# Kernel tuning notes

Hardware: AMD Instinct MI355X
Metric: run time of the kernel (lower is better)

## Reference

```python
import jax, jax.numpy as jnp
import numpy as np

WSZ = 8
HEADS = 8
FILTER_RATE = 0.3
EPS = 1e-5


def layer_norm(x, w, b):
    mu = x.mean(-1, keepdims=True)
    var = ((x - mu) ** 2).mean(-1, keepdims=True)
    return (x - mu) * jax.lax.rsqrt(var + EPS) * w + b


def setup_inputs() -> dict:
    key = jax.random.key(0)
    ks = jax.random.split(key, 8)
    B, C, H, W = 2, 256, 512, 512
    C2 = 2 * C
    s = 0.02
    return {
        "feature_map": jax.random.normal(ks[0], (B, C, H, W), jnp.float32),
        "uncertain_map": jax.random.uniform(ks[1], (B, H, W), jnp.float32),
        "norm_w": jnp.ones((C,), jnp.float32),
        "norm_b": jnp.zeros((C,), jnp.float32),
        "lin0_w": jax.random.normal(ks[2], (C, C2), jnp.float32) * s,
        "lin0_b": jnp.zeros((C2,), jnp.float32),
        "qkv0_w": jax.random.normal(ks[3], (C2, 3 * C2), jnp.float32) * s,
        "lin1_w": jax.random.normal(ks[4], (C2, C2), jnp.float32) * s,
        "lin1_b": jnp.zeros((C2,), jnp.float32),
        "qkv1_w": jax.random.normal(ks[5], (C2, 3 * C2), jnp.float32) * s,
        "proj_w": jax.random.normal(ks[6], (C2, C), jnp.float32) * s,
        "proj_b": jnp.zeros((C,), jnp.float32),
    }


def _window_attn(xf, qkv_w, scale, winsz, C2):
    # xf: (N, winsz, C2)
    qkv = (xf @ qkv_w).reshape(-1, winsz, 3, HEADS, C2 // HEADS)
    q, k, v = qkv[:, :, 0], qkv[:, :, 1], qkv[:, :, 2]  # (N, winsz, H, dh)
    a = jnp.einsum("nqhd,nkhd->nhqk", q, k) * scale
    a = jax.nn.softmax(a, axis=-1)
    o = jnp.einsum("nhqk,nkhd->nqhd", a, v).reshape(-1, winsz, C2)
    return xf + o


def reference(feature_map, uncertain_map, norm_w, norm_b, lin0_w, lin0_b,
              qkv0_w, lin1_w, lin1_b, qkv1_w, proj_w, proj_b):
    B, C, H, W = feature_map.shape
    wsz = WSZ
    nH, nW = H // wsz, W // wsz
    nWin, winsz = nH * nW, wsz * wsz
    nWF = int(nWin * FILTER_RATE)
    C2 = 2 * C
    scale = (C // HEADS) ** -0.5  # module uses C//num_heads, not C2//num_heads

    # window partition
    x = jnp.transpose(feature_map, (0, 2, 3, 1))  # B H W C
    win_x = x.reshape(B, nH, wsz, nW, wsz, C).transpose(0, 1, 3, 2, 4, 5)
    win_x = win_x.reshape(B * nWin, winsz, C)
    win_unc = uncertain_map.reshape(B, nH, wsz, nW, wsz).transpose(0, 1, 3, 2, 4)
    win_unc = win_unc.reshape(B, nWin, winsz)

    # topk window selection by mean uncertainty
    score = win_unc.mean(-1)  # (B, nWin)
    _, idx = jax.lax.top_k(score, nWF)  # (B, nWF)
    flat_idx = (idx + jnp.arange(B)[:, None] * nWin).reshape(-1)  # (B*nWF,)

    xw = win_x[flat_idx]  # gather: (B*nWF, winsz, C)
    xn = layer_norm(xw, norm_w, norm_b)

    # local branch: repeat 0
    xf = jax.nn.gelu(xn @ lin0_w + lin0_b, approximate=False)
    xf = _window_attn(xf, qkv0_w, scale, winsz, C2)
    # repeat 1
    xf = xf + jax.nn.gelu(xf @ lin1_w + lin1_b, approximate=False)
    xf = _window_attn(xf, qkv1_w, scale, winsz, C2)

    out_f = xn + jax.nn.gelu(xf @ proj_w + proj_b, approximate=False)

    # scatter-add back into unnormalized windows
    win_x = win_x.at[flat_idx].add(out_f)

    x = win_x.reshape(B, nH, nW, wsz, wsz, C).transpose(0, 1, 3, 2, 4, 5)
    x = x.reshape(B, H, W, C)
    return jnp.transpose(x, (0, 3, 1, 2))
```

## Files before the change

kernel.cpp:

```cpp
#include <hip/hip_runtime.h>
#include <math.h>

typedef unsigned short u16;
typedef unsigned int   u32;
typedef __attribute__((ext_vector_type(8))) short bf16x8;
typedef __attribute__((ext_vector_type(4))) float f32x4;

#define DEV static __device__ __forceinline__

DEV u16 f2b(float f) {
  union { float f; u32 u; } v; v.f = f;
  u32 r = v.u + 0x7FFFu + ((v.u >> 16) & 1u);
  return (u16)(r >> 16);
}
DEV float b2f(u16 h) {
  union { u32 u; float f; } v; v.u = ((u32)h) << 16;
  return v.f;
}
DEV float gelu_f(float x) { return 0.5f * x * (1.0f + erff(x * 0.70710678118654752f)); }

DEV void gload16(const u16* g, u16* l) {
  __builtin_amdgcn_global_load_lds(
      (const __attribute__((address_space(1))) void*)g,
      (__attribute__((address_space(3))) void*)l, 16, 0, 0);
}

__global__ void k_transpose_w(const float* __restrict__ src, u16* __restrict__ dst,
                              int K, int N) {
  long t = (long)blockIdx.x * 256 + threadIdx.x;
  if (t >= (long)K * N) return;
  int n = (int)(t / K), k = (int)(t % K);
  dst[t] = f2b(src[(long)k * N + n]);
}

__global__ void k_scores(const float* __restrict__ unc, float* __restrict__ scores) {
  int id = blockIdx.x * 256 + threadIdx.x;
  if (id >= 8192) return;
  int b = id >> 12, win = id & 4095;
  int h0 = (win >> 6) << 3, w0 = (win & 63) << 3;
  float r[8] = {0.f,0.f,0.f,0.f,0.f,0.f,0.f,0.f};
  for (int i = 0; i < 8; ++i) {
    long base = ((long)(b * 512 + h0 + i)) * 512 + w0;
    #pragma unroll
    for (int j = 0; j < 8; ++j) r[j] += unc[base + j];
  }
  float s = ((r[0] + r[1]) + (r[2] + r[3])) + ((r[4] + r[5]) + (r[6] + r[7]));
  scores[id] = s * (1.0f / 64.0f);
}

__global__ __launch_bounds__(1024) void k_topk(
    const float* __restrict__ scores, int* __restrict__ row2win,
    int* __restrict__ win2row, int nWF) {
  __shared__ float ls[4096];
  __shared__ int   li[4096];
  const int b = blockIdx.x;
  const int tid = threadIdx.x;
  for (int i = tid; i < 4096; i += 1024) {
    ls[i] = scores[b * 4096 + i];
    li[i] = i;
    win2row[b * 4096 + i] = -1;
  }
  __syncthreads();
  for (int k = 2; k <= 4096; k <<= 1) {
    for (int j = k >> 1; j > 0; j >>= 1) {
      for (int t = tid; t < 2048; t += 1024) {
        int i = ((t / j) * (j << 1)) + (t % j);
        int ixj = i + j;
        bool up = ((i & k) == 0);
        float sa = ls[i], sb = ls[ixj];
        int ia = li[i], ib = li[ixj];
        bool g = (sa > sb) || (sa == sb && ia < ib);
        if (g != up) { ls[i] = sb; ls[ixj] = sa; li[i] = ib; li[ixj] = ia; }
      }
      __syncthreads();
    }
  }
  for (int r = tid; r < nWF; r += 1024) {
    int win = li[r];
    row2win[b * nWF + r] = (b << 12) | win;
    win2row[b * 4096 + win] = b * nWF + r;
  }
}

__global__ __launch_bounds__(256) void k_gather_ln(
    const float* __restrict__ fm, const float* __restrict__ nw,
    const float* __restrict__ nb, const int* __restrict__ row2win,
    u16* __restrict__ xn, int winStart) {
  __shared__ float sx[64 * 256];
  const int tid = threadIdx.x;
  const int rw = row2win[winStart + blockIdx.x];
  const int b = rw >> 12, win = rw & 4095;
  const int h0 = (win >> 6) << 3, w0 = (win & 63) << 3;
  {
    const int c8 = tid >> 3, h = tid & 7;
    #pragma unroll
    for (int cc = 0; cc < 8; ++cc) {
      const int c = cc * 32 + c8;
      long base = ((long)(b * 256 + c) * 512 + h0 + h) * 512 + w0;
      float4 v0 = *(const float4*)(fm + base);
      float4 v1 = *(const float4*)(fm + base + 4);
      float vv[8] = {v0.x, v0.y, v0.z, v0.w, v1.x, v1.y, v1.z, v1.w};
      #pragma unroll
      for (int j = 0; j < 8; ++j) {
        int tok = h * 8 + j;
        sx[tok * 256 + (c ^ ((tok & 15) << 1))] = vv[j];
      }
    }
  }
  __syncthreads();
  const int tok = tid >> 2, g = tid & 3;
  const int swz = (tok & 15) << 1;
  float sum = 0.f;
  for (int q = 0; q < 64; ++q) sum += sx[tok * 256 + ((g * 64 + q) ^ swz)];
  sum += __shfl_xor(sum, 1);
  sum += __shfl_xor(sum, 2);
  const float mu = sum * (1.0f / 256.0f);
  float s2 = 0.f;
  for (int q = 0; q < 64; ++q) {
    float d = sx[tok * 256 + ((g * 64 + q) ^ swz)] - mu;
    s2 += d * d;
  }
  s2 += __shfl_xor(s2, 1);
  s2 += __shfl_xor(s2, 2);
  const float rs = rsqrtf(s2 * (1.0f / 256.0f) + 1e-5f);
  long obase = ((long)blockIdx.x * 64 + tok) * 256 + g * 64;
  for (int q8 = 0; q8 < 8; ++q8) {
    u16 tmp[8];
    #pragma unroll
    for (int e = 0; e < 8; ++e) {
      int c = g * 64 + q8 * 8 + e;
      float v = (sx[tok * 256 + (c ^ swz)] - mu) * rs * nw[c] + nb[c];
      tmp[e] = f2b(v);
    }
    *(ulonglong2*)(xn + obase + q8 * 8) = *(const ulonglong2*)tmp;
  }
}

template <int EPI, int NT, int KD>
__global__ __launch_bounds__(512, 2) void k_gemm256(
    const u16* __restrict__ A, const u16* __restrict__ Bt,
    const float* __restrict__ bias, const u16* __restrict__ Res,
    u16* __restrict__ Y, int N) {
  __shared__ __attribute__((aligned(16))) u16 S[65536];
  const int tid = threadIdx.x;
  const int l = tid & 63, wid = tid >> 6;
  const int wm = wid >> 2, wn = wid & 3;

  const int nwg = gridDim.x;
  const int d = blockIdx.x;
  const int xcd = d & 7, j = d >> 3;
  const int q = nwg >> 3, r8 = nwg & 7;
  const int wrk = (xcd < r8 ? xcd * (q + 1) : r8 * (q + 1) + (xcd - r8) * q) + j;
  const int tm = wrk / NT, tn = wrk % NT;

  const int srow = wid * 8 + (l >> 3);
  const int k0b = ((l & 7) << 4) ^ ((l >> 3) << 4);
  const u16* gA = A + (long)(tm * 256 + srow) * KD + (k0b >> 1);
  const u16* gB = Bt + (long)(tn * 256 + srow) * KD + (k0b >> 1);
  char* ldsS = (char*)S + wid * 1024 + l * 16;
  const char* Sb = (const char*)S;

  f32x4 acc[8][4] = {};
  bf16x8 bfrag[4][2];
  bf16x8 af[2][2];

#define STG(T, ISB, H) do { \
    const u16* g_ = (ISB) ? gB : gA; \
    char* lp_ = ldsS + ((T) & 1) * 65536 + (ISB) * 32768 + (H) * 16384; \
    gload16(g_ + (long)((H) * 128) * KD + (long)(T) * 64, (u16*)lp_); \
    gload16(g_ + (long)((H) * 128 + 64) * KD + (long)(T) * 64, (u16*)(lp_ + 8192)); \
  } while (0)

#define DS_B(T) do { \
    _Pragma("unroll") for (int ni_ = 0; ni_ < 4; ++ni_) { \
      const int r_ = wn * 64 + ni_ * 16 + (l & 15); \
      _Pragma("unroll") for (int kk_ = 0; kk_ < 2; ++kk_) { \
        const int kb_ = kk_ * 64 + ((l >> 4) << 4); \
        bfrag[ni_][kk_] = *(const bf16x8*)(Sb + ((T) & 1) * 65536 + 32768 + r_ * 128 + (kb_ ^ ((r_ & 7) << 4))); \
      } } \
  } while (0)

#define DS_A(T, Q) do { \
    _Pragma("unroll") for (int m2_ = 0; m2_ < 2; ++m2_) { \
      const int r_ = wm * 128 + (2 * (Q) + m2_) * 16 + (l & 15); \
      _Pragma("unroll") for (int kk_ = 0; kk_ < 2; ++kk_) { \
        const int kb_ = kk_ * 64 + ((l >> 4) << 4); \
        af[m2_][kk_] = *(const bf16x8*)(Sb + ((T) & 1) * 65536 + r_ * 128 + (kb_ ^ ((r_ & 7) << 4))); \
      } } \
  } while (0)

#define MFMA16(Q) do { \
    _Pragma("unroll") for (int m2_ = 0; m2_ < 2; ++m2_) \
      _Pragma("unroll") for (int ni_ = 0; ni_ < 4; ++ni_) \
        _Pragma("unroll") for (int kk_ = 0; kk_ < 2; ++kk_) \
          acc[2 * (Q) + m2_][ni_] = __builtin_amdgcn_mfma_f32_16x16x32_bf16( \
              af[m2_][kk_], bfrag[ni_][kk_], acc[2 * (Q) + m2_][ni_], 0, 0, 0); \
  } while (0)

#define BAR_MFMA(Q) do { \
    __builtin_amdgcn_s_barrier(); \
    asm volatile("s_waitcnt lgkmcnt(0)" ::: "memory"); \
    __builtin_amdgcn_sched_barrier(0); \
    __builtin_amdgcn_s_setprio(1); \
    MFMA16(Q); \
    __builtin_amdgcn_s_setprio(0); \
  } while (0)

#define PH_END() do { \
    __builtin_amdgcn_s_barrier(); \
    __builtin_amdgcn_sched_barrier(0); \
  } while (0)

  STG(0, 0, 0); STG(0, 0, 1); STG(0, 1, 0); STG(0, 1, 1);
  STG(1, 0, 0); STG(1, 0, 1); STG(1, 1, 0); STG(1, 1, 1);
  asm volatile("s_waitcnt vmcnt(8)" ::: "memory");
  __builtin_amdgcn_s_barrier();
  __builtin_amdgcn_sched_barrier(0);

  constexpr int nIter = KD >> 7;
  for (int i = 0; i < nIter; ++i) {
    const int t0 = 2 * i, t1 = 2 * i + 1;
    const bool more = (i + 1 < nIter);
    DS_B(t0); DS_A(t0, 0);
    if (i > 0) STG(t1, 0, 0);
    BAR_MFMA(0); PH_END();
    DS_A(t0, 1);
    if (i > 0) STG(t1, 0, 1);
    if (more) STG(t0 + 2, 1, 0);
    BAR_MFMA(1); PH_END();
    DS_A(t0, 2);
    if (more) STG(t0 + 2, 1, 1);
    BAR_MFMA(2); PH_END();
    DS_A(t0, 3);
    BAR_MFMA(3);
    if (more) { asm volatile("s_waitcnt vmcnt(4)" ::: "memory"); }
    else      { asm volatile("s_waitcnt vmcnt(0)" ::: "memory"); }
    PH_END();
    DS_B(t1); DS_A(t1, 0);
    if (more) STG(t0 + 2, 0, 0);
    BAR_MFMA(0); PH_END();
    DS_A(t1, 1);
    if (more) STG(t0 + 2, 0, 1);
    BAR_MFMA(1); PH_END();
    DS_A(t1, 2);
    if (more) STG(t1 + 2, 1, 0);
    BAR_MFMA(2); PH_END();
    DS_A(t1, 3);
    if (more) STG(t1 + 2, 1, 1);
    BAR_MFMA(3);
    if (more) { asm volatile("s_waitcnt vmcnt(4)" ::: "memory"); }
    PH_END();
  }

  if (EPI == 3) {
    float bv[4];
    #pragma unroll
    for (int ni = 0; ni < 4; ++ni)
      bv[ni] = bias[tn * 256 + wn * 64 + ni * 16 + (l & 15)];
    #pragma unroll
    for (int mi = 0; mi < 8; ++mi) {
      #pragma unroll
      for (int r = 0; r < 4; ++r) {
        const int ml = wm * 128 + mi * 16 + ((l >> 4) << 2) + r;
        #pragma unroll
        for (int ni = 0; ni < 4; ++ni) {
          const int nl = wn * 64 + ni * 16 + (l & 15);
          float v = gelu_f(acc[mi][ni][r] + bv[ni]);
          S[nl * 256 + ((((ml >> 3) ^ ((nl & 7) << 2)) << 3) | (ml & 7))] = f2b(v);
        }
      }
    }
    asm volatile("s_waitcnt lgkmcnt(0)" ::: "memory");
    __builtin_amdgcn_s_barrier();
    #pragma unroll
    for (int rd = 0; rd < 16; ++rd) {
      const int id = rd * 512 + tid;
      const int nl = id >> 5, c8 = id & 31;
      ulonglong2 val = *(const ulonglong2*)(S + nl * 256 + ((c8 ^ ((nl & 7) << 2)) << 3));
      u16 tv[8];
      *(ulonglong2*)tv = val;
      const long mg = (long)tm * 256 + c8 * 8;
      const int ng = tn * 256 + nl;
      #pragma unroll
      for (int e = 0; e < 8; ++e) tv[e] = f2b(b2f(tv[e]) + b2f(Res[(mg + e) * N + ng]));
      const long row = (mg >> 6);
      *(ulonglong2*)(Y + (row * 256 + ng) * 64 + (c8 & 7) * 8) = *(const ulonglong2*)tv;
    }
  } else {
    float bv[4];
    if (EPI == 1 || EPI == 2) {
      #pragma unroll
      for (int ni = 0; ni < 4; ++ni)
        bv[ni] = bias[tn * 256 + wn * 64 + ni * 16 + (l & 15)];
    }
    #pragma unroll
    for (int sw = 0; sw < 4; ++sw) {
      #pragma unroll
      for (int mi2 = 0; mi2 < 2; ++mi2) {
        const int mi = 2 * sw + mi2;
        const int lr0 = wm * 32 + mi2 * 16 + ((l >> 4) << 2);
        #pragma unroll
        for (int r = 0; r < 4; ++r) {
          const int lrr = lr0 + r;
          #pragma unroll
          for (int ni = 0; ni < 4; ++ni) {
            float v = acc[mi][ni][r];
            if (EPI == 1 || EPI == 2) v = gelu_f(v + bv[ni]);
            const int col = wn * 64 + ni * 16 + (l & 15);
            S[lrr * 256 + ((((col >> 3) ^ (lrr & 7)) << 3) | (col & 7))] = f2b(v);
          }
        }
      }
      asm volatile("s_waitcnt lgkmcnt(0)" ::: "memory");
      __builtin_amdgcn_s_barrier();
      const int lr2 = tid >> 3;
      const long m = (long)tm * 256 + (lr2 >> 5) * 128 + sw * 32 + (lr2 & 31);
      #pragma unroll
      for (int rd = 0; rd < 4; ++rd) {
        const int chunk = rd * 8 + (tid & 7);
        ulonglong2 val = *(const ulonglong2*)(S + lr2 * 256 + ((chunk ^ (lr2 & 7)) << 3));
        const int n = tn * 256 + chunk * 8;
        if (EPI == 2) {
          u16 tv[8], rv[8];
          *(ulonglong2*)tv = val;
          *(ulonglong2*)rv = *(const ulonglong2*)(Res + m * N + n);
          #pragma unroll
          for (int e = 0; e < 8; ++e) tv[e] = f2b(b2f(tv[e]) + b2f(rv[e]));
          val = *(const ulonglong2*)tv;
        }
        if (EPI == 4) {
          const long win = m >> 6;
          const int t_ = n >> 9, h_ = (n >> 6) & 7, d0 = n & 63;
          *(ulonglong2*)(Y + ((((win * 8 + h_) * 3 + t_) * 64 + (m & 63)) * 64 + d0)) = val;
        } else {
          *(ulonglong2*)(Y + m * N + n) = val;
        }
      }
      if (sw < 3) {
        __builtin_amdgcn_s_barrier();
      }
    }
  }
#undef STG
#undef DS_B
#undef DS_A
#undef MFMA16
#undef BAR_MFMA
#undef PH_END
}

__global__ __launch_bounds__(256) void k_attn(
    const u16* __restrict__ qkv, u16* __restrict__ xf) {
  __shared__ __attribute__((aligned(16))) u16 sq[64 * 64];
  __shared__ __attribute__((aligned(16))) u16 sk[64 * 64];
  __shared__ __attribute__((aligned(16))) u16 sv[64 * 64];
  __shared__ __attribute__((aligned(16))) u16 sp[64 * 64];
  const int tid = threadIdx.x;
  const int l = tid & 63, w = tid >> 6;
  const int wloc = blockIdx.x >> 3, h = blockIdx.x & 7;
  const long tokbase = (long)wloc * 64;
  const u16* base = qkv + (long)blockIdx.x * 12288;

  #pragma unroll
  for (int rd = 0; rd < 6; ++rd) {
    const int cid = rd * 256 + tid;
    ulonglong2 v16 = *(const ulonglong2*)(base + (long)cid * 8);
    const int t = (cid >> 3) & 63, d0 = (cid & 7) << 3;
    if (rd < 2) {
      *(ulonglong2*)((char*)sq + t * 128 + ((d0 * 2) ^ ((t & 7) << 4))) = v16;
    } else if (rd < 4) {
      *(ulonglong2*)((char*)sk + t * 128 + ((d0 * 2) ^ ((t & 7) << 4))) = v16;
    } else {
      u16 vv[8];
      *(ulonglong2*)vv = v16;
      #pragma unroll
      for (int e = 0; e < 8; ++e) {
        int r = d0 + e;
        *(u16*)((char*)sv + r * 128 + ((t * 2) ^ ((r & 7) << 4))) = vv[e];
      }
    }
  }
  __syncthreads();

  f32x4 accs[4] = {};
  #pragma unroll
  for (int ks = 0; ks < 2; ++ks) {
    int kb = ks * 64 + ((l >> 4) << 4);
    int ra = w * 16 + (l & 15);
    bf16x8 aq = *(const bf16x8*)((char*)sq + ra * 128 + (kb ^ ((ra & 7) << 4)));
    #pragma unroll
    for (int cf = 0; cf < 4; ++cf) {
      int rb = cf * 16 + (l & 15);
      bf16x8 bk = *(const bf16x8*)((char*)sk + rb * 128 + (kb ^ ((rb & 7) << 4)));
      accs[cf] = __builtin_amdgcn_mfma_f32_16x16x32_bf16(aq, bk, accs[cf], 0, 0, 0);
    }
  }
  const float scale = 0.17677669529663687f;
  float pv[4][4];
  #pragma unroll
  for (int r = 0; r < 4; ++r) {
    float m = -1e30f;
    #pragma unroll
    for (int cf = 0; cf < 4; ++cf) {
      pv[cf][r] = accs[cf][r] * scale;
      m = fmaxf(m, pv[cf][r]);
    }
    for (int off = 1; off < 16; off <<= 1) m = fmaxf(m, __shfl_xor(m, off));
    float s = 0.f;
    #pragma unroll
    for (int cf = 0; cf < 4; ++cf) { pv[cf][r] = __expf(pv[cf][r] - m); s += pv[cf][r]; }
    for (int off = 1; off < 16; off <<= 1) s += __shfl_xor(s, off);
    float inv = 1.0f / s;
    #pragma unroll
    for (int cf = 0; cf < 4; ++cf) pv[cf][r] *= inv;
  }
  #pragma unroll
  for (int cf = 0; cf < 4; ++cf)
    #pragma unroll
    for (int r = 0; r < 4; ++r) {
      int pr = w * 16 + ((l >> 4) << 2) + r, pc = cf * 16 + (l & 15);
      *(u16*)((char*)sp + pr * 128 + ((pc * 2) ^ ((pr & 7) << 4))) = f2b(pv[cf][r]);
    }
  __syncthreads();

  f32x4 acco[4] = {};
  #pragma unroll
  for (int ks = 0; ks < 2; ++ks) {
    int kb = ks * 64 + ((l >> 4) << 4);
    int ra = w * 16 + (l & 15);
    bf16x8 ap = *(const bf16x8*)((char*)sp + ra * 128 + (kb ^ ((ra & 7) << 4)));
    #pragma unroll
    for (int cf = 0; cf < 4; ++cf) {
      int rb = cf * 16 + (l & 15);
      bf16x8 bvv = *(const bf16x8*)((char*)sv + rb * 128 + (kb ^ ((rb & 7) << 4)));
      acco[cf] = __builtin_amdgcn_mfma_f32_16x16x32_bf16(ap, bvv, acco[cf], 0, 0, 0);
    }
  }
  #pragma unroll
  for (int cf = 0; cf < 4; ++cf)
    #pragma unroll
    for (int r = 0; r < 4; ++r) {
      int orow = w * 16 + ((l >> 4) << 2) + r, ocol = cf * 16 + (l & 15);
      *(u16*)((char*)sq + orow * 128 + ((ocol * 2) ^ ((orow & 7) << 4))) = f2b(acco[cf][r]);
    }
  __syncthreads();
  {
    const int row = tid >> 2, c32 = tid & 3;
    const long gaddr = (tokbase + row) * 512 + h * 64 + c32 * 16;
    #pragma unroll
    for (int hh = 0; hh < 2; ++hh) {
      const int colb = c32 * 32 + hh * 16;
      ulonglong2 ov = *(const ulonglong2*)((char*)sq + row * 128 + (colb ^ ((row & 7) << 4)));
      ulonglong2 xv = *(const ulonglong2*)(xf + gaddr + hh * 8);
      u16 o16[8], x16[8];
      *(ulonglong2*)o16 = ov;
      *(ulonglong2*)x16 = xv;
      #pragma unroll
      for (int e = 0; e < 8; ++e) x16[e] = f2b(b2f(x16[e]) + b2f(o16[e]));
      *(ulonglong2*)(xf + gaddr + hh * 8) = *(const ulonglong2*)x16;
    }
  }
}

__global__ __launch_bounds__(256) void k_assemble(
    const float* __restrict__ fm, const u16* __restrict__ out_f,
    const int* __restrict__ win2row, float* __restrict__ out) {
  const int tid = threadIdx.x;
  const int bq = blockIdx.x;
  const int hw = bq & 63, c = (bq >> 6) & 255, b = bq >> 14;
  const int w0 = (tid & 127) << 2;
  const int hlo = tid >> 7;
  const int win = hw * 64 + (w0 >> 3);
  const int r = win2row[b * 4096 + win];
  const u16* ofb = out_f + ((long)(r < 0 ? 0 : r) * 256 + c) * 64 + (w0 & 7);
  const long base = ((long)(b * 256 + c) * 512 + hw * 8) * 512 + w0;
  #pragma unroll
  for (int jj = 0; jj < 4; ++jj) {
    const int h = jj * 2 + hlo;
    float4 v = *(const float4*)(fm + base + (long)h * 512);
    if (r >= 0) {
      ushort4 ov = *(const ushort4*)(ofb + h * 8);
      v.x += b2f(ov.x);
      v.y += b2f(ov.y);
      v.z += b2f(ov.z);
      v.w += b2f(ov.w);
    }
    *(float4*)(out + base + (long)h * 512) = v;
  }
}

extern "C" void kernel_launch(void* const* d_in, const int* in_sizes, int n_in,
                              void* d_out, int out_size, void* d_ws, size_t ws_size,
                              hipStream_t stream) {
  const float* fm     = (const float*)d_in[0];
  const float* unc    = (const float*)d_in[1];
  const float* nw     = (const float*)d_in[2];
  const float* nb     = (const float*)d_in[3];
  const float* w_lin0 = (const float*)d_in[4];
  const float* b_lin0 = (const float*)d_in[5];
  const float* w_qkv0 = (const float*)d_in[6];
  const float* w_lin1 = (const float*)d_in[7];
  const float* b_lin1 = (const float*)d_in[8];
  const float* w_qkv1 = (const float*)d_in[9];
  const float* w_proj = (const float*)d_in[10];
  const float* b_proj = (const float*)d_in[11];
  float* out = (float*)d_out;

  const int nWF = 1228, totWin = 2456;
  const long totTok = (long)totWin * 64;

  char* p = (char*)d_ws;
  auto alloc = [&](size_t bytes) {
    char* r = p;
    p += (bytes + 255) & ~(size_t)255;
    return r;
  };
  float* scores = (float*)alloc(8192 * 4);
  int* win2row  = (int*)alloc(8192 * 4);
  int* row2win  = (int*)alloc(totWin * 4);
  u16* wT       = (u16*)alloc((size_t)2097152 * 2);
  u16* out_f    = (u16*)alloc((size_t)(totTok + 256) * 256 * 2);
  size_t persist = (size_t)(p - (char*)d_ws);

  int wpc = totWin;
  {
    const int cands[6] = {1, 2, 4, 8, 16, 32};
    for (int ci = 0; ci < 6; ++ci) {
      int n = cands[ci];
      int wp = ((totWin + n - 1) / n + 3) & ~3;
      size_t mc = (size_t)wp * 64;
      size_t need = persist + 4096 +
                    ((mc * 256 * 2 + 255) & ~(size_t)255) +
                    2 * ((mc * 512 * 2 + 255) & ~(size_t)255) +
                    ((mc * 1536 * 2 + 255) & ~(size_t)255);
      if (need <= ws_size) { wpc = wp; break; }
    }
  }
  long mcap = (long)wpc * 64;
  u16* xn   = (u16*)alloc((size_t)mcap * 256 * 2);
  u16* xfa  = (u16*)alloc((size_t)mcap * 512 * 2);
  u16* xfb  = (u16*)alloc((size_t)mcap * 512 * 2);
  u16* qkvb = (u16*)alloc((size_t)mcap * 1536 * 2);

  u16* wT_lin0 = wT;
  u16* wT_qkv0 = wT + 131072;
  u16* wT_lin1 = wT + 917504;
  u16* wT_qkv1 = wT + 1179648;
  u16* wT_proj = wT + 1966080;
  k_transpose_w<<<(131072 + 255) / 256, 256, 0, stream>>>(w_lin0, wT_lin0, 256, 512);
  k_transpose_w<<<(786432 + 255) / 256, 256, 0, stream>>>(w_qkv0, wT_qkv0, 512, 1536);
  k_transpose_w<<<(262144 + 255) / 256, 256, 0, stream>>>(w_lin1, wT_lin1, 512, 512);
  k_transpose_w<<<(786432 + 255) / 256, 256, 0, stream>>>(w_qkv1, wT_qkv1, 512, 1536);
  k_transpose_w<<<(131072 + 255) / 256, 256, 0, stream>>>(w_proj, wT_proj, 512, 256);

  k_scores<<<32, 256, 0, stream>>>(unc, scores);
  k_topk<<<2, 1024, 0, stream>>>(scores, row2win, win2row, nWF);

  for (int w0 = 0; w0 < totWin; w0 += wpc) {
    int rem = totWin - w0;
    int wn = (wpc < rem) ? wpc : rem;
    int mT = wn / 4;
    k_gather_ln<<<wn, 256, 0, stream>>>(fm, nw, nb, row2win, xn, w0);
    k_gemm256<1, 2, 256><<<mT * 2, 512, 0, stream>>>(xn, wT_lin0, b_lin0, nullptr, xfa, 512);
    k_gemm256<4, 6, 512><<<mT * 6, 512, 0, stream>>>(xfa, wT_qkv0, nullptr, nullptr, qkvb, 1536);
    k_attn<<<wn * 8, 256, 0, stream>>>(qkvb, xfa);
    k_gemm256<2, 2, 512><<<mT * 2, 512, 0, stream>>>(xfa, wT_lin1, b_lin1, xfa, xfb, 512);
    k_gemm256<4, 6, 512><<<mT * 6, 512, 0, stream>>>(xfb, wT_qkv1, nullptr, nullptr, qkvb, 1536);
    k_attn<<<wn * 8, 256, 0, stream>>>(qkvb, xfb);
    k_gemm256<3, 1, 512><<<mT * 1, 512, 0, stream>>>(xfb, wT_proj, b_proj, xn,
                                                     out_f + (long)w0 * 16384, 256);
  }
  k_assemble<<<32768, 256, 0, stream>>>(fm, out_f, win2row, out);
}
```

Baseline: 1.759 ms.

## Process paired N-tiles per GEMM block with in-loop epilogue and trim attention LDS

The GEMM kernel gains a PAIR parameter so each workgroup computes two adjacent 256-wide N tiles back to back. The K-tile pipeline runs continuously across both tiles, and the epilogue for the first tile runs inside the loop using a separate LDS buffer E, so prefetch of the next tile's operands can overlap with it. The A-tile is re-read from global for the second N tile, and the grid is halved. The attention kernel drops its separate P buffer by reusing the K buffer after QK^T, and defers the V transpose into LDS until after the softmax, holding V in registers. This lowers LDS use at the cost of an extra barrier. The larger GEMM LDS footprint may reduce occupancy, and fewer workgroups may underfill the GPU.

```diff
diff --git a/kernel.cpp b/kernel.cpp
--- a/kernel.cpp
+++ b/kernel.cpp
@@ -136,12 +136,16 @@
   }
 }
 
-template <int EPI, int NT, int KD>
+template <int EPI, int NT, int KD, int PAIR>
 __global__ __launch_bounds__(512, 2) void k_gemm256(
     const u16* __restrict__ A, const u16* __restrict__ Bt,
     const float* __restrict__ bias, const u16* __restrict__ Res,
     u16* __restrict__ Y, int N) {
+  constexpr int NKT = KD / 64;
+  constexpr int LG_NKT = (KD == 512) ? 3 : 2;
+  constexpr int NIP = KD / 128;
   __shared__ __attribute__((aligned(16))) u16 S[65536];
+  __shared__ __attribute__((aligned(16))) u16 E[16384];
   const int tid = threadIdx.x;
   const int l = tid & 63, wid = tid >> 6;
   const int wm = wid >> 2, wn = wid & 3;
@@ -151,12 +155,13 @@
   const int xcd = d & 7, j = d >> 3;
   const int q = nwg >> 3, r8 = nwg & 7;
   const int wrk = (xcd < r8 ? xcd * (q + 1) : r8 * (q + 1) + (xcd - r8) * q) + j;
-  const int tm = wrk / NT, tn = wrk % NT;
+  constexpr int NTP = NT / PAIR;
+  const int tm = wrk / NTP, tp = wrk % NTP;
 
   const int srow = wid * 8 + (l >> 3);
   const int k0b = ((l & 7) << 4) ^ ((l >> 3) << 4);
-  const u16* gA = A + (long)(tm * 256 + srow) * KD + (k0b >> 1);
-  const u16* gB = Bt + (long)(tn * 256 + srow) * KD + (k0b >> 1);
+  const int vko = k0b >> 1;
+  const u16* gA = A + (long)(tm * 256 + srow) * KD + vko;
   char* ldsS = (char*)S + wid * 1024 + l * 16;
   const char* Sb = (const char*)S;
 
@@ -164,11 +169,18 @@
   bf16x8 bfrag[4][2];
   bf16x8 af[2][2];
 
-#define STG(T, ISB, H) do { \
-    const u16* g_ = (ISB) ? gB : gA; \
-    char* lp_ = ldsS + ((T) & 1) * 65536 + (ISB) * 32768 + (H) * 16384; \
-    gload16(g_ + (long)((H) * 128) * KD + (long)(T) * 64, (u16*)lp_); \
-    gload16(g_ + (long)((H) * 128 + 64) * KD + (long)(T) * 64, (u16*)(lp_ + 8192)); \
+#define STG(G, ISB, H) do { \
+    const int ktg_ = (G) & (NKT - 1); \
+    const u16* g_; \
+    if (ISB) { \
+      const int tng_ = tp * PAIR + ((G) >> LG_NKT); \
+      g_ = Bt + (long)(tng_ * 256 + srow) * KD + vko; \
+    } else { \
+      g_ = gA; \
+    } \
+    char* lp_ = ldsS + ((G) & 1) * 65536 + (ISB) * 32768 + (H) * 16384; \
+    gload16(g_ + (long)((H) * 128) * KD + ktg_ * 64, (u16*)lp_); \
+    gload16(g_ + (long)((H) * 128 + 64) * KD + ktg_ * 64, (u16*)(lp_ + 8192)); \
   } while (0)
 
 #define DS_B(T) do { \
@@ -217,7 +229,7 @@
   __builtin_amdgcn_s_barrier();
   __builtin_amdgcn_sched_barrier(0);
 
-  constexpr int nIter = KD >> 7;
+  constexpr int nIter = (PAIR * NKT) >> 1;
   for (int i = 0; i < nIter; ++i) {
     const int t0 = 2 * i, t1 = 2 * i + 1;
     const bool more = (i + 1 < nIter);
@@ -250,95 +262,101 @@
     BAR_MFMA(3);
     if (more) { asm volatile("s_waitcnt vmcnt(4)" ::: "memory"); }
     PH_END();
-  }
-
-  if (EPI == 3) {
-    float bv[4];
-    #pragma unroll
-    for (int ni = 0; ni < 4; ++ni)
-      bv[ni] = bias[tn * 256 + wn * 64 + ni * 16 + (l & 15)];
-    #pragma unroll
-    for (int mi = 0; mi < 8; ++mi) {
-      #pragma unroll
-      for (int r = 0; r < 4; ++r) {
-        const int ml = wm * 128 + mi * 16 + ((l >> 4) << 2) + r;
+
+    if (((i + 1) & (NIP - 1)) == 0) {
+      const int tn = tp * PAIR + ((i + 1) / NIP - 1);
+      if (EPI == 3) {
+        float bv[4];
         #pragma unroll
-        for (int ni = 0; ni < 4; ++ni) {
-          const int nl = wn * 64 + ni * 16 + (l & 15);
-          float v = gelu_f(acc[mi][ni][r] + bv[ni]);
-          S[nl * 256 + ((((ml >> 3) ^ ((nl & 7) << 2)) << 3) | (ml & 7))] = f2b(v);
+        for (int ni = 0; ni < 4; ++ni)
+          bv[ni] = bias[tn * 256 + wn * 64 + ni * 16 + (l & 15)];
+        #pragma unroll
+        for (int mi = 0; mi < 8; ++mi) {
+          #pragma unroll
+          for (int r = 0; r < 4; ++r) {
+            const int ml = wm * 128 + mi * 16 + ((l >> 4) << 2) + r;
+            #pragma unroll
+            for (int ni = 0; ni < 4; ++ni) {
+              const int nl = wn * 64 + ni * 16 + (l & 15);
+              float v = gelu_f(acc[mi][ni][r] + bv[ni]);
+              S[nl * 256 + ((((ml >> 3) ^ ((nl & 7) << 2)) << 3) | (ml & 7))] = f2b(v);
+            }
+          }
+        }
+        asm volatile("s_waitcnt lgkmcnt(0)" ::: "memory");
+        __builtin_amdgcn_s_barrier();
+        #pragma unroll
+        for (int rd = 0; rd < 16; ++rd) {
+          const int id = rd * 512 + tid;
+          const int nl = id >> 5, c8 = id & 31;
+          ulonglong2 val = *(const ulonglong2*)(S + nl * 256 + ((c8 ^ ((nl & 7) << 2)) << 3));
+          u16 tv[8];
+          *(ulonglong2*)tv = val;
+          const long mg = (long)tm * 256 + c8 * 8;
+          const int ng = tn * 256 + nl;
+          #pragma unroll
+          for (int e = 0; e < 8; ++e) tv[e] = f2b(b2f(tv[e]) + b2f(Res[(mg + e) * N + ng]));
+          const long row = (mg >> 6);
+          *(ulonglong2*)(Y + (row * 256 + ng) * 64 + (c8 & 7) * 8) = *(const ulonglong2*)tv;
+        }
+      } else {
+        float bv[4];
+        if (EPI == 1 || EPI == 2) {
+          #pragma unroll
+          for (int ni = 0; ni < 4; ++ni)
+            bv[ni] = bias[tn * 256 + wn * 64 + ni * 16 + (l & 15)];
+        }
+        #pragma unroll
+        for (int sw = 0; sw < 4; ++sw) {
+          #pragma unroll
+          for (int mi2 = 0; mi2 < 2; ++mi2) {
+            const int mi = 2 * sw + mi2;
+            const int lr0 = wm * 32 + mi2 * 16 + ((l >> 4) << 2);
+            #pragma unroll
+            for (int r = 0; r < 4; ++r) {
+              const int lrr = lr0 + r;
+              #pragma unroll
+              for (int ni = 0; ni < 4; ++ni) {
+                float v = acc[mi][ni][r];
+                if (EPI == 1 || EPI == 2) v = gelu_f(v + bv[ni]);
+                const int col = wn * 64 + ni * 16 + (l & 15);
+                E[lrr * 256 + ((((col >> 3) ^ (lrr & 7)) << 3) | (col & 7))] = f2b(v);
+              }
+            }
+          }
+          asm volatile("s_waitcnt lgkmcnt(0)" ::: "memory");
+          __builtin_amdgcn_s_barrier();
+          const int lr2 = tid >> 3;
+          const long m = (long)tm * 256 + (lr2 >> 5) * 128 + sw * 32 + (lr2 & 31);
+          #pragma unroll
+          for (int rd = 0; rd < 4; ++rd) {
+            const int chunk = rd * 8 + (tid & 7);
+            ulonglong2 val = *(const ulonglong2*)(E + lr2 * 256 + ((chunk ^ (lr2 & 7)) << 3));
+            const int n = tn * 256 + chunk * 8;
+            if (EPI == 2) {
+              u16 tv[8], rv[8];
+              *(ulonglong2*)tv = val;
+              *(ulonglong2*)rv = *(const ulonglong2*)(Res + m * N + n);
+              #pragma unroll
+              for (int e = 0; e < 8; ++e) tv[e] = f2b(b2f(tv[e]) + b2f(rv[e]));
+              val = *(const ulonglong2*)tv;
+            }
+            if (EPI == 4) {
+              const long win = m >> 6;
+              const int t_ = n >> 9, h_ = (n >> 6) & 7, d0 = n & 63;
+              *(ulonglong2*)(Y + ((((win * 8 + h_) * 3 + t_) * 64 + (m & 63)) * 64 + d0)) = val;
+            } else {
+              *(ulonglong2*)(Y + m * N + n) = val;
+            }
+          }
+          __builtin_amdgcn_s_barrier();
         }
       }
-    }
-    asm volatile("s_waitcnt lgkmcnt(0)" ::: "memory");
-    __builtin_amdgcn_s_barrier();
-    #pragma unroll
-    for (int rd = 0; rd < 16; ++rd) {
-      const int id = rd * 512 + tid;
-      const int nl = id >> 5, c8 = id & 31;
-      ulonglong2 val = *(const ulonglong2*)(S + nl * 256 + ((c8 ^ ((nl & 7) << 2)) << 3));
-      u16 tv[8];
-      *(ulonglong2*)tv = val;
-      const long mg = (long)tm * 256 + c8 * 8;
-      const int ng = tn * 256 + nl;
       #pragma unroll
-      for (int e = 0; e < 8; ++e) tv[e] = f2b(b2f(tv[e]) + b2f(Res[(mg + e) * N + ng]));
-      const long row = (mg >> 6);
-      *(ulonglong2*)(Y + (row * 256 + ng) * 64 + (c8 & 7) * 8) = *(const ulonglong2*)tv;
-    }
-  } else {
-    float bv[4];
-    if (EPI == 1 || EPI == 2) {
-      #pragma unroll
-      for (int ni = 0; ni < 4; ++ni)
-        bv[ni] = bias[tn * 256 + wn * 64 + ni * 16 + (l & 15)];
-    }
-    #pragma unroll
-    for (int sw = 0; sw < 4; ++sw) {
-      #pragma unroll
-      for (int mi2 = 0; mi2 < 2; ++mi2) {
-        const int mi = 2 * sw + mi2;
-        const int lr0 = wm * 32 + mi2 * 16 + ((l >> 4) << 2);
+      for (int mi = 0; mi < 8; ++mi)
         #pragma unroll
-        for (int r = 0; r < 4; ++r) {
-          const int lrr = lr0 + r;
-          #pragma unroll
-          for (int ni = 0; ni < 4; ++ni) {
-            float v = acc[mi][ni][r];
-            if (EPI == 1 || EPI == 2) v = gelu_f(v + bv[ni]);
-            const int col = wn * 64 + ni * 16 + (l & 15);
-            S[lrr * 256 + ((((col >> 3) ^ (lrr & 7)) << 3) | (col & 7))] = f2b(v);
-          }
-        }
-      }
-      asm volatile("s_waitcnt lgkmcnt(0)" ::: "memory");
-      __builtin_amdgcn_s_barrier();
-      const int lr2 = tid >> 3;
-      const long m = (long)tm * 256 + (lr2 >> 5) * 128 + sw * 32 + (lr2 & 31);
-      #pragma unroll
-      for (int rd = 0; rd < 4; ++rd) {
-        const int chunk = rd * 8 + (tid & 7);
-        ulonglong2 val = *(const ulonglong2*)(S + lr2 * 256 + ((chunk ^ (lr2 & 7)) << 3));
-        const int n = tn * 256 + chunk * 8;
-        if (EPI == 2) {
-          u16 tv[8], rv[8];
-          *(ulonglong2*)tv = val;
-          *(ulonglong2*)rv = *(const ulonglong2*)(Res + m * N + n);
-          #pragma unroll
-          for (int e = 0; e < 8; ++e) tv[e] = f2b(b2f(tv[e]) + b2f(rv[e]));
-          val = *(const ulonglong2*)tv;
-        }
-        if (EPI == 4) {
-          const long win = m >> 6;
-          const int t_ = n >> 9, h_ = (n >> 6) & 7, d0 = n & 63;
-          *(ulonglong2*)(Y + ((((win * 8 + h_) * 3 + t_) * 64 + (m & 63)) * 64 + d0)) = val;
-        } else {
-          *(ulonglong2*)(Y + m * N + n) = val;
-        }
-      }
-      if (sw < 3) {
-        __builtin_amdgcn_s_barrier();
-      }
+        for (int ni = 0; ni < 4; ++ni)
+          acc[mi][ni] = (f32x4){0.f, 0.f, 0.f, 0.f};
     }
   }
 #undef STG
@@ -354,31 +372,23 @@
   __shared__ __attribute__((aligned(16))) u16 sq[64 * 64];
   __shared__ __attribute__((aligned(16))) u16 sk[64 * 64];
   __shared__ __attribute__((aligned(16))) u16 sv[64 * 64];
-  __shared__ __attribute__((aligned(16))) u16 sp[64 * 64];
   const int tid = threadIdx.x;
   const int l = tid & 63, w = tid >> 6;
   const int wloc = blockIdx.x >> 3, h = blockIdx.x & 7;
   const long tokbase = (long)wloc * 64;
   const u16* base = qkv + (long)blockIdx.x * 12288;
 
-  #pragma unroll
-  for (int rd = 0; rd < 6; ++rd) {
+  ulonglong2 vreg[2];
+  vreg[0] = *(const ulonglong2*)(base + (long)(1024 + tid) * 8);
+  vreg[1] = *(const ulonglong2*)(base + (long)(1280 + tid) * 8);
+  #pragma unroll
+  for (int rd = 0; rd < 4; ++rd) {
     const int cid = rd * 256 + tid;
     ulonglong2 v16 = *(const ulonglong2*)(base + (long)cid * 8);
     const int t = (cid >> 3) & 63, d0 = (cid & 7) << 3;
-    if (rd < 2) {
-      *(ulonglong2*)((char*)sq + t * 128 + ((d0 * 2) ^ ((t & 7) << 4))) = v16;
-    } else if (rd < 4) {
-      *(ulonglong2*)((char*)sk + t * 128 + ((d0 * 2) ^ ((t & 7) << 4))) = v16;
-    } else {
-      u16 vv[8];
-      *(ulonglong2*)vv = v16;
-      #pragma unroll
-      for (int e = 0; e < 8; ++e) {
-        int r = d0 + e;
-        *(u16*)((char*)sv + r * 128 + ((t * 2) ^ ((r & 7) << 4))) = vv[e];
-      }
-    }
+    const int sbyte = t * 128 + ((d0 * 2) ^ ((t & 7) << 4));
+    if (rd < 2) *(ulonglong2*)((char*)sq + sbyte) = v16;
+    else        *(ulonglong2*)((char*)sk + sbyte) = v16;
   }
   __syncthreads();
 
@@ -395,6 +405,8 @@
       accs[cf] = __builtin_amdgcn_mfma_f32_16x16x32_bf16(aq, bk, accs[cf], 0, 0, 0);
     }
   }
+  __syncthreads();
+
   const float scale = 0.17677669529663687f;
   float pv[4][4];
   #pragma unroll
@@ -419,8 +431,20 @@
     #pragma unroll
     for (int r = 0; r < 4; ++r) {
       int pr = w * 16 + ((l >> 4) << 2) + r, pc = cf * 16 + (l & 15);
-      *(u16*)((char*)sp + pr * 128 + ((pc * 2) ^ ((pr & 7) << 4))) = f2b(pv[cf][r]);
-    }
+      *(u16*)((char*)sk + pr * 128 + ((pc * 2) ^ ((pr & 7) << 4))) = f2b(pv[cf][r]);
+    }
+  #pragma unroll
+  for (int rv = 0; rv < 2; ++rv) {
+    const int cid = (4 + rv) * 256 + tid;
+    const int t = (cid >> 3) & 63, d0 = (cid & 7) << 3;
+    u16 vv[8];
+    *(ulonglong2*)vv = vreg[rv];
+    #pragma unroll
+    for (int e = 0; e < 8; ++e) {
+      int r = d0 + e;
+      *(u16*)((char*)sv + r * 128 + ((t * 2) ^ ((r & 7) << 4))) = vv[e];
+    }
+  }
   __syncthreads();
 
   f32x4 acco[4] = {};
@@ -428,7 +452,7 @@
   for (int ks = 0; ks < 2; ++ks) {
     int kb = ks * 64 + ((l >> 4) << 4);
     int ra = w * 16 + (l & 15);
-    bf16x8 ap = *(const bf16x8*)((char*)sp + ra * 128 + (kb ^ ((ra & 7) << 4)));
+    bf16x8 ap = *(const bf16x8*)((char*)sk + ra * 128 + (kb ^ ((ra & 7) << 4)));
     #pragma unroll
     for (int cf = 0; cf < 4; ++cf) {
       int rb = cf * 16 + (l & 15);
@@ -561,14 +585,14 @@
     int wn = (wpc < rem) ? wpc : rem;
     int mT = wn / 4;
     k_gather_ln<<<wn, 256, 0, stream>>>(fm, nw, nb, row2win, xn, w0);
-    k_gemm256<1, 2, 256><<<mT * 2, 512, 0, stream>>>(xn, wT_lin0, b_lin0, nullptr, xfa, 512);
-    k_gemm256<4, 6, 512><<<mT * 6, 512, 0, stream>>>(xfa, wT_qkv0, nullptr, nullptr, qkvb, 1536);
+    k_gemm256<1, 2, 256, 2><<<mT * 1, 512, 0, stream>>>(xn, wT_lin0, b_lin0, nullptr, xfa, 512);
+    k_gemm256<4, 6, 512, 2><<<mT * 3, 512, 0, stream>>>(xfa, wT_qkv0, nullptr, nullptr, qkvb, 1536);
     k_attn<<<wn * 8, 256, 0, stream>>>(qkvb, xfa);
-    k_gemm256<2, 2, 512><<<mT * 2, 512, 0, stream>>>(xfa, wT_lin1, b_lin1, xfa, xfb, 512);
-    k_gemm256<4, 6, 512><<<mT * 6, 512, 0, stream>>>(xfb, wT_qkv1, nullptr, nullptr, qkvb, 1536);
+    k_gemm256<2, 2, 512, 2><<<mT * 1, 512, 0, stream>>>(xfa, wT_lin1, b_lin1, xfa, xfb, 512);
+    k_gemm256<4, 6, 512, 2><<<mT * 3, 512, 0, stream>>>(xfb, wT_qkv1, nullptr, nullptr, qkvb, 1536);
     k_attn<<<wn * 8, 256, 0, stream>>>(qkvb, xfb);
-    k_gemm256<3, 1, 512><<<mT * 1, 512, 0, stream>>>(xfb, wT_proj, b_proj, xn,
-                                                     out_f + (long)w0 * 16384, 256);
+    k_gemm256<3, 1, 512, 1><<<mT * 1, 512, 0, stream>>>(xfb, wT_proj, b_proj, xn,
+                                                        out_f + (long)w0 * 16384, 256);
   }
   k_assemble<<<32768, 256, 0, stream>>>(fm, out_f, win2row, out);
 }
```

New measurement: 2.011 ms. +14.3%, slower.
